# Kernel tuning notes

Measured on AMD Instinct MI355X. Metric: run time of the kernel, lower is better.

Reference implementation:

```python
import jax, jax.numpy as jnp
import numpy as np

D_MODEL = 1024
N_HEADS = 16
D_K = D_MODEL // N_HEADS


def setup_inputs() -> dict:
    key = jax.random.key(0)
    ks = jax.random.split(key, 16)
    B, S = 2, 2048
    sc = 1.0 / np.sqrt(D_MODEL)
    inp = {
        "query": jax.random.normal(ks[0], (B, S, D_MODEL), jnp.float32),
        "key": jax.random.normal(ks[1], (B, S, D_MODEL), jnp.float32),
        "value": jax.random.normal(ks[2], (B, S, D_MODEL), jnp.float32),
        "Wq": jax.random.normal(ks[3], (D_MODEL, D_MODEL), jnp.float32) * sc,
        "bq": jnp.zeros((D_MODEL,), jnp.float32),
        "Wk": jax.random.normal(ks[4], (D_MODEL, D_MODEL), jnp.float32) * sc,
        "bk": jnp.zeros((D_MODEL,), jnp.float32),
        "Wv": jax.random.normal(ks[5], (D_MODEL, D_MODEL), jnp.float32) * sc,
        "bv": jnp.zeros((D_MODEL,), jnp.float32),
        "Wo": jax.random.normal(ks[6], (D_MODEL, D_MODEL), jnp.float32) * sc,
        "bo": jnp.zeros((D_MODEL,), jnp.float32),
        "theta": jax.random.normal(ks[7], (N_HEADS,), jnp.float32) * 0.1,
        "gate": jax.random.normal(ks[8], (D_MODEL,), jnp.float32) * 0.1,
    }
    return inp


def reference(query, key, value, Wq, bq, Wk, bk, Wv, bv, Wo, bo, theta, gate):
    B, Sq, D = query.shape
    Sk = key.shape[1]
    # linear projections (torch Linear: x @ W.T + b), split heads -> [B,H,S,d_k]
    Q = (query @ Wq.T + bq).reshape(B, Sq, N_HEADS, D_K).transpose(0, 2, 1, 3)
    K = (key @ Wk.T + bk).reshape(B, Sk, N_HEADS, D_K).transpose(0, 2, 1, 3)
    V = (value @ Wv.T + bv).reshape(B, Sk, N_HEADS, D_K).transpose(0, 2, 1, 3)

    inv_sqrt_dk = 1.0 / jnp.sqrt(jnp.float32(D_K))
    scores = jnp.einsum("bhqd,bhkd->bhqk", Q, K) * inv_sqrt_dk

    # per-head rotation of the first two feature dims of Q
    cos_t = jnp.cos(theta)[None, :, None, None]  # [1,H,1,1]
    sin_t = jnp.sin(theta)[None, :, None, None]
    q_rot = jnp.concatenate(
        [
            cos_t * Q[..., :1] - sin_t * Q[..., 1:2],
            sin_t * Q[..., :1] + cos_t * Q[..., 1:2],
            Q[..., 2:],
        ],
        axis=-1,
    )
    scores_q = jnp.einsum("bhqd,bhkd->bhqk", q_rot, K) * inv_sqrt_dk

    g_scalar = jax.nn.sigmoid(gate.mean())
    scores = g_scalar * scores_q + (1.0 - g_scalar) * scores

    attn = jax.nn.softmax(scores, axis=-1)
    out = jnp.einsum("bhqk,bhkd->bhqd", attn, V)
    out = out.transpose(0, 2, 1, 3).reshape(B, Sq, D)
    return out @ Wo.T + bo
```

## Files before the change

### kernel.cpp

```cpp
#include <hip/hip_runtime.h>


typedef __bf16 bf16;
typedef __attribute__((ext_vector_type(8))) bf16 bf16x8;
typedef __attribute__((ext_vector_type(4))) bf16 bf16x4;
typedef __attribute__((ext_vector_type(2))) bf16 bf16x2;
typedef __attribute__((ext_vector_type(4))) float f32x4;
typedef unsigned int u32;

#define D_MODEL 1024
#define NH 16
#define DKH 64
#define SEQ 2048

#define GLL16(g, l) __builtin_amdgcn_global_load_lds(                      \
    (const __attribute__((address_space(1))) void*)(g),                    \
    (__attribute__((address_space(3))) void*)(l), 16, 0, 0)

static __device__ __forceinline__ f32x4 mfma16(bf16x8 a, bf16x8 b, f32x4 c) {
  return __builtin_amdgcn_mfma_f32_16x16x32_bf16(a, b, c, 0, 0, 0);
}

static __device__ __forceinline__ u32 pk2(float a, float b) {
  bf16x2 v; v[0] = (bf16)a; v[1] = (bf16)b;
  return __builtin_bit_cast(u32, v);
}

static __device__ __forceinline__ float fexp2(float x) {
#if __has_builtin(__builtin_amdgcn_exp2f)
  return __builtin_amdgcn_exp2f(x);
#else
  return exp2f(x);
#endif
}

#define CQK 0.1803368801111244f
#define MSHIFT 12.0f

__global__ __launch_bounds__(256) void prep(const float* __restrict__ query,
                                            const float* __restrict__ key,
                                            const float* __restrict__ value,
                                            const float* __restrict__ Wq,
                                            const float* __restrict__ bq,
                                            const float* __restrict__ Wk,
                                            const float* __restrict__ Wv,
                                            const float* __restrict__ Wo,
                                            const float* __restrict__ gate,
                                            const float* __restrict__ theta,
                                            bf16* __restrict__ Xq,
                                            bf16* __restrict__ Xk,
                                            bf16* __restrict__ Xv,
                                            bf16* __restrict__ Wqp,
                                            bf16* __restrict__ Wkp,
                                            bf16* __restrict__ Wvp,
                                            bf16* __restrict__ Wop,
                                            float* __restrict__ bqp) {
  const int id = blockIdx.x;
  const int tid = threadIdx.x;
  if (id >= 4096) {
    const int rem = id - 4096;
    const int iz = rem >> 12;
    const int ib = rem & 4095;
    const float* s = (iz == 0) ? query : (iz == 1) ? key : value;
    bf16* d = (iz == 0) ? Xq : (iz == 1) ? Xk : Xv;
    const size_t i = (size_t)(ib * 256 + tid) * 4;
    float4 w = *(const float4*)(s + i);
    bf16x4 o; o[0] = (bf16)w.x; o[1] = (bf16)w.y; o[2] = (bf16)w.z; o[3] = (bf16)w.w;
    *(bf16x4*)(d + i) = o;
    return;
  }
  const int wz = id >> 10, wb = id & 1023;
  if (wz != 0) {
    const float* s = (wz == 1) ? Wk : (wz == 2) ? Wv : Wo;
    bf16* dd = (wz == 1) ? Wkp : (wz == 2) ? Wvp : Wop;
    const size_t i = (size_t)(wb * 256 + tid) * 4;
    float4 v = *(const float4*)(s + i);
    bf16x4 o4; o4[0] = (bf16)v.x; o4[1] = (bf16)v.y; o4[2] = (bf16)v.z; o4[3] = (bf16)v.w;
    *(bf16x4*)(dd + i) = o4;
    return;
  }
  __shared__ float red[4];
  float ssum = 0.f;
  for (int i = tid; i < D_MODEL; i += 256) ssum += gate[i];
#pragma unroll
  for (int off = 32; off > 0; off >>= 1) ssum += __shfl_down(ssum, off);
  if ((tid & 63) == 0) red[tid >> 6] = ssum;
  __syncthreads();
  const float g = 1.f / (1.f + __expf(-(red[0] + red[1] + red[2] + red[3]) / 1024.f));

  const int t = wb * 256 + tid;
  const int r = t >> 8;
  const int c0 = (t & 255) * 4;
  const int d = r & 63, h = r >> 6;
  float4 w = *(const float4*)(Wq + (size_t)r * D_MODEL + c0);
  float4 o;
  if (d == 0) {
    const float a = (g * cosf(theta[h]) + (1.f - g)) * CQK;
    const float bb = (g * sinf(theta[h])) * CQK;
    float4 w2 = *(const float4*)(Wq + (size_t)(r + 1) * D_MODEL + c0);
    o.x = a * w.x - bb * w2.x; o.y = a * w.y - bb * w2.y;
    o.z = a * w.z - bb * w2.z; o.w = a * w.w - bb * w2.w;
    if (c0 == 0) bqp[r] = a * bq[r] - bb * bq[r + 1];
  } else if (d == 1) {
    const float a = (g * cosf(theta[h]) + (1.f - g)) * CQK;
    const float bb = (g * sinf(theta[h])) * CQK;
    float4 w2 = *(const float4*)(Wq + (size_t)(r - 1) * D_MODEL + c0);
    o.x = bb * w2.x + a * w.x; o.y = bb * w2.y + a * w.y;
    o.z = bb * w2.z + a * w.z; o.w = bb * w2.w + a * w.w;
    if (c0 == 0) bqp[r] = bb * bq[r - 1] + a * bq[r];
  } else {
    o.x = CQK * w.x; o.y = CQK * w.y;
    o.z = CQK * w.z; o.w = CQK * w.w;
    if (c0 == 0) bqp[r] = CQK * bq[r];
  }
  bf16x4 ov; ov[0] = (bf16)o.x; ov[1] = (bf16)o.y; ov[2] = (bf16)o.z; ov[3] = (bf16)o.w;
  *(bf16x4*)(Wqp + (size_t)r * D_MODEL + c0) = ov;
}

static __device__ __forceinline__ void gemm_bt_main(const bf16* __restrict__ A,
                                                    const bf16* __restrict__ Bt,
                                                    int tm, int tn, int K,
                                                    f32x4 acc[4][4]) {
  __shared__ bf16 lA[8192];
  __shared__ bf16 lB[8192];
  const int tid = threadIdx.x;
  const int lane = tid & 63, wv = tid >> 6;
  const int wm = wv >> 1, wn = wv & 1;
  const int l16 = lane & 15, lg = lane >> 4;

#pragma unroll
  for (int i = 0; i < 4; ++i)
#pragma unroll
    for (int j = 0; j < 4; ++j) acc[i][j] = (f32x4){0.f, 0.f, 0.f, 0.f};

  int offA[4][2], offB[4][2];
#pragma unroll
  for (int f = 0; f < 4; ++f)
#pragma unroll
    for (int kc = 0; kc < 2; ++kc) {
      const int m = wm * 64 + f * 16 + l16;
      offA[f][kc] = m * 64 + (((kc * 4 + lg) ^ (m & 7)) << 3);
      const int n = wn * 64 + f * 16 + l16;
      offB[f][kc] = n * 64 + (((kc * 4 + lg) ^ (n & 7)) << 3);
    }

  const int rowb = tid >> 3, oct = tid & 7;
  const int soct = oct ^ (rowb & 7);
  const bf16* gA[4];
  const bf16* gB[4];
#pragma unroll
  for (int rd = 0; rd < 4; ++rd) {
    gA[rd] = A + (size_t)(tm + rd * 32 + rowb) * K + soct * 8;
    gB[rd] = Bt + (size_t)(tn + rd * 32 + rowb) * K + soct * 8;
  }

  for (int kt = 0; kt < K; kt += 64) {
    __syncthreads();
#pragma unroll
    for (int rd = 0; rd < 4; ++rd) {
      GLL16(gA[rd] + kt, &lA[rd * 2048 + wv * 512]);
      GLL16(gB[rd] + kt, &lB[rd * 2048 + wv * 512]);
    }
    __syncthreads();
#pragma unroll
    for (int kc = 0; kc < 2; ++kc) {
      bf16x8 af[4], bv[4];
#pragma unroll
      for (int f = 0; f < 4; ++f) {
        af[f] = *(const bf16x8*)&lA[offA[f][kc]];
        bv[f] = *(const bf16x8*)&lB[offB[f][kc]];
      }
#pragma unroll
      for (int i = 0; i < 4; ++i)
#pragma unroll
        for (int j = 0; j < 4; ++j)
          acc[i][j] = mfma16(af[i], bv[j], acc[i][j]);
    }
  }
}

__global__ __launch_bounds__(256) void gemm_qkv(
    const bf16* __restrict__ Xq, const bf16* __restrict__ Xk, const bf16* __restrict__ Xv,
    const bf16* __restrict__ Wq, const bf16* __restrict__ Wk, const bf16* __restrict__ Wv,
    const float* __restrict__ bqp, const float* __restrict__ bk, const float* __restrict__ bv,
    bf16* __restrict__ Qp, bf16* __restrict__ Kp, bf16* __restrict__ Vt) {
  const int wgp = (blockIdx.x & 7) * 96 + (blockIdx.x >> 3);
  const int z = wgp >> 8;
  const int rem = wgp & 255;
  const int tm = (rem >> 3) * 128, tn = (rem & 7) * 128;
  const bf16* A = (z == 0) ? Xq : (z == 1) ? Xk : Xv;
  const bf16* Bt = (z == 0) ? Wq : (z == 1) ? Wk : Wv;
  const float* bias = (z == 0) ? bqp : (z == 1) ? bk : bv;
  f32x4 acc[4][4];
  gemm_bt_main(A, Bt, tm, tn, D_MODEL, acc);
  const int lane = threadIdx.x & 63, wv = threadIdx.x >> 6;
  const int wm = wv >> 1, wn = wv & 1, l16 = lane & 15, lg = lane >> 4;
  if (z < 2) {
    bf16* C = (z == 0) ? Qp : Kp;
#pragma unroll
    for (int i = 0; i < 4; ++i) {
      const int m0 = tm + wm * 64 + i * 16 + lg * 4;
#pragma unroll
      for (int j = 0; j < 4; ++j) {
        const int n = tn + wn * 64 + j * 16 + l16;
        const float bb = bias[n];
        const int h = n >> 6, d = n & 63;
#pragma unroll
        for (int r = 0; r < 4; ++r) {
          const int m = m0 + r;
          const int b = m >> 11, s = m & 2047;
          C[((size_t)(b * NH + h) * SEQ + s) * DKH + d] = (bf16)(acc[i][j][r] + bb);
        }
      }
    }
  } else {
#pragma unroll
    for (int i = 0; i < 4; ++i) {
      const int m0 = tm + wm * 64 + i * 16 + lg * 4;
      const int b = m0 >> 11, s0 = m0 & 2047;
#pragma unroll
      for (int j = 0; j < 4; ++j) {
        const int n = tn + wn * 64 + j * 16 + l16;
        const float bb = bias[n];
        const int h = n >> 6, d = n & 63;
        bf16x4 ov;
#pragma unroll
        for (int r = 0; r < 4; ++r) ov[r] = (bf16)(acc[i][j][r] + bb);
        *(bf16x4*)&Vt[((size_t)(b * NH + h) * DKH + d) * SEQ + s0] = ov;
      }
    }
  }
}

__global__ __launch_bounds__(256) void gemm_out_k(const bf16* __restrict__ A,
                                                  const bf16* __restrict__ Bt,
                                                  const float* __restrict__ bias,
                                                  float* __restrict__ C) {
  const int wgp = (blockIdx.x & 7) * 32 + (blockIdx.x >> 3);
  const int tm = (wgp >> 3) * 128, tn = (wgp & 7) * 128;
  f32x4 acc[4][4];
  gemm_bt_main(A, Bt, tm, tn, D_MODEL, acc);
  const int lane = threadIdx.x & 63, wv = threadIdx.x >> 6;
  const int wm = wv >> 1, wn = wv & 1, l16 = lane & 15, lg = lane >> 4;
#pragma unroll
  for (int i = 0; i < 4; ++i) {
    const int m0 = tm + wm * 64 + i * 16 + lg * 4;
#pragma unroll
    for (int j = 0; j < 4; ++j) {
      const int n = tn + wn * 64 + j * 16 + l16;
      const float bb = bias[n];
#pragma unroll
      for (int r = 0; r < 4; ++r)
        C[(size_t)(m0 + r) * D_MODEL + n] = acc[i][j][r] + bb;
    }
  }
}

__global__ __launch_bounds__(512, 4) void attn_kernel(const bf16* __restrict__ Qp,
                                                      const bf16* __restrict__ Kp,
                                                      const bf16* __restrict__ Vt,
                                                      bf16* __restrict__ Op) {
  __shared__ __align__(16) char smem[81920];
  bf16 (*lK)[8192] = (bf16(*)[8192])smem;
  bf16 (*lV)[8192] = (bf16(*)[8192])(smem + 32768);
  bf16* lP = (bf16*)(smem + 65536);
  float* cmb = (float*)smem;
  float* cl  = (float*)(smem + 65536);

  const int tid = threadIdx.x;
  const int lane = tid & 63, w = tid >> 6;
  const int l16 = lane & 15, lg = lane >> 4;
  const int qg = w >> 1, kg = w & 1;
  const int wgp = (blockIdx.x & 7) * 64 + (blockIdx.x >> 3);
  const int bh = wgp >> 4;
  const int b = bh >> 4, h = bh & 15;
  const int q0 = (wgp & 15) * 128;
  const int qw0 = q0 + qg * 32;
  const size_t kvb = (size_t)bh * SEQ * DKH;

  bf16x8 aq[2][2];
#pragma unroll
  for (int qq = 0; qq < 2; ++qq)
#pragma unroll
    for (int kc = 0; kc < 2; ++kc)
      aq[qq][kc] = *(const bf16x8*)&Qp[kvb +
          (size_t)(qw0 + qq * 16 + l16) * DKH + kc * 32 + lg * 8];

  f32x4 o[2][4];
#pragma unroll
  for (int qq = 0; qq < 2; ++qq)
#pragma unroll
    for (int dt = 0; dt < 4; ++dt) o[qq][dt] = (f32x4){0.f, 0.f, 0.f, 0.f};
  f32x4 lacc[2];
  lacc[0] = (f32x4){0.f, 0.f, 0.f, 0.f};
  lacc[1] = (f32x4){0.f, 0.f, 0.f, 0.f};

  bf16x8 ones;
#pragma unroll
  for (int j = 0; j < 8; ++j) ones[j] = (bf16)1.0f;

  const int kr = tid >> 3, oct = tid & 7;
  const bf16* gK = Kp + kvb + (size_t)kr * DKH + (oct ^ (kr & 7)) * 8;
  const int kswz0 = kr * 64 + (oct << 3);
  const int kswz1 = (kr + 64) * 64 + (oct << 3);
  const int vd = tid >> 4, vsc = tid & 15;
  const bf16* gV = Vt + kvb + (size_t)vd * SEQ + vsc * 8;
  const int vswz0 = vd * 128 + ((vsc ^ (vd & 7)) << 3);
  const int vswz1 = (vd + 32) * 128 + ((vsc ^ (vd & 7)) << 3);

  bf16* lPw = &lP[w * 1024];
  int pwr[2][2];
#pragma unroll
  for (int fn = 0; fn < 2; ++fn)
#pragma unroll
    for (int qq = 0; qq < 2; ++qq)
      pwr[fn][qq] = l16 * 64 + (((qq * 4 + fn * 2 + (lg >> 1)) ^ (l16 & 7)) << 3) +
                    ((lg & 1) << 2);
  int prd[2];
#pragma unroll
  for (int qq = 0; qq < 2; ++qq)
    prd[qq] = l16 * 64 + (((qq * 4 + lg) ^ (l16 & 7)) << 3);

  bf16x8 k0r = *(const bf16x8*)(gK);
  bf16x8 k1r = *(const bf16x8*)(gK + (size_t)64 * DKH);
  bf16x8 v0r = *(const bf16x8*)(gV);
  bf16x8 v1r = *(const bf16x8*)(gV + (size_t)32 * SEQ);
  *(bf16x8*)&lK[0][kswz0] = k0r;  *(bf16x8*)&lK[0][kswz1] = k1r;
  *(bf16x8*)&lV[0][vswz0] = v0r;  *(bf16x8*)&lV[0][vswz1] = v1r;
  k0r = *(const bf16x8*)(gK + (size_t)128 * DKH);
  k1r = *(const bf16x8*)(gK + (size_t)192 * DKH);
  v0r = *(const bf16x8*)(gV + 128);
  v1r = *(const bf16x8*)(gV + (size_t)32 * SEQ + 128);
  __syncthreads();

  const int NT = SEQ / 128;
  for (int t = 0; t < NT; ++t) {
    const bf16* K = &lK[t & 1][0];
    const bf16* V = &lV[t & 1][0];

#pragma unroll
    for (int ss = 0; ss < 2; ++ss) {
      f32x4 st[2][2];
      __builtin_amdgcn_s_setprio(1);
#pragma unroll
      for (int fn = 0; fn < 2; ++fn) {
        const int row = ss * 64 + kg * 32 + fn * 16 + l16;
        bf16x8 ka = *(const bf16x8*)&K[row * 64 + ((lg ^ (row & 7)) << 3)];
        bf16x8 kb = *(const bf16x8*)&K[row * 64 + (((4 + lg) ^ (row & 7)) << 3)];
#pragma unroll
        for (int qq = 0; qq < 2; ++qq) {
          f32x4 tt = (f32x4){0.f, 0.f, 0.f, 0.f};
          tt = mfma16(ka, aq[qq][0], tt);
          tt = mfma16(kb, aq[qq][1], tt);
          st[fn][qq] = tt;
        }
      }
      __builtin_amdgcn_s_setprio(0);

#pragma unroll
      for (int fn = 0; fn < 2; ++fn)
#pragma unroll
        for (int qq = 0; qq < 2; ++qq) {
          uint2 pw;
          pw.x = pk2(fexp2(st[fn][qq][0] - MSHIFT), fexp2(st[fn][qq][1] - MSHIFT));
          pw.y = pk2(fexp2(st[fn][qq][2] - MSHIFT), fexp2(st[fn][qq][3] - MSHIFT));
          *(uint2*)&lPw[pwr[fn][qq]] = pw;
        }

      bf16x8 pa0 = *(const bf16x8*)&lPw[prd[0]];
      bf16x8 pa1 = *(const bf16x8*)&lPw[prd[1]];

      __builtin_amdgcn_s_setprio(1);
      lacc[0] = mfma16(pa0, ones, lacc[0]);
      lacc[1] = mfma16(pa1, ones, lacc[1]);
#pragma unroll
      for (int dt = 0; dt < 4; ++dt) {
        const int n = dt * 16 + l16;
        bf16x8 vv = *(const bf16x8*)&V[n * 128 +
                                      (((ss * 8 + kg * 4 + lg) ^ (n & 7)) << 3)];
        o[0][dt] = mfma16(pa0, vv, o[0][dt]);
        o[1][dt] = mfma16(pa1, vv, o[1][dt]);
      }
      __builtin_amdgcn_s_setprio(0);
    }

    if (t + 1 < NT) {
      const int nb = (t + 1) & 1;
      *(bf16x8*)&lK[nb][kswz0] = k0r;  *(bf16x8*)&lK[nb][kswz1] = k1r;
      *(bf16x8*)&lV[nb][vswz0] = v0r;  *(bf16x8*)&lV[nb][vswz1] = v1r;
      if (t + 2 < NT) {
        const int kt2 = (t + 2) * 128;
        k0r = *(const bf16x8*)(gK + (size_t)kt2 * DKH);
        k1r = *(const bf16x8*)(gK + (size_t)(kt2 + 64) * DKH);
        v0r = *(const bf16x8*)(gV + kt2);
        v1r = *(const bf16x8*)(gV + (size_t)32 * SEQ + kt2);
      }
    }
    __syncthreads();
  }

  if (kg == 1) {
#pragma unroll
    for (int qq = 0; qq < 2; ++qq)
#pragma unroll
      for (int dt = 0; dt < 4; ++dt)
        *(f32x4*)&cmb[(size_t)qg * 2048 + ((qq * 4 + dt) * 16 + l16) * 16 + lg * 4] =
            o[qq][dt];
    if (l16 == 0) {
#pragma unroll
      for (int qq = 0; qq < 2; ++qq)
#pragma unroll
        for (int r = 0; r < 4; ++r)
          cl[(qg * 2 + qq) * 16 + lg * 4 + r] = lacc[qq][r];
    }
  }
  __syncthreads();
  if (kg == 0) {
#pragma unroll
    for (int qq = 0; qq < 2; ++qq) {
#pragma unroll
      for (int dt = 0; dt < 4; ++dt) {
        f32x4 p = *(const f32x4*)&cmb[(size_t)qg * 2048 +
                                      ((qq * 4 + dt) * 16 + l16) * 16 + lg * 4];
        o[qq][dt][0] += p[0]; o[qq][dt][1] += p[1];
        o[qq][dt][2] += p[2]; o[qq][dt][3] += p[3];
      }
      float linv[4];
#pragma unroll
      for (int r = 0; r < 4; ++r)
        linv[r] = 1.f / (lacc[qq][r] + cl[(qg * 2 + qq) * 16 + lg * 4 + r]);
#pragma unroll
      for (int r = 0; r < 4; ++r) {
        const int q = qw0 + qq * 16 + lg * 4 + r;
#pragma unroll
        for (int dt = 0; dt < 4; ++dt) {
          const int d = dt * 16 + l16;
          Op[((size_t)(b * SEQ + q)) * D_MODEL + h * DKH + d] =
              (bf16)(o[qq][dt][r] * linv[r]);
        }
      }
    }
  }
}

extern "C" void kernel_launch(void* const* d_in, const int* in_sizes, int n_in,
                              void* d_out, int out_size, void* d_ws, size_t ws_size,
                              hipStream_t stream) {
  (void)in_sizes; (void)n_in; (void)out_size; (void)ws_size;
  const float* query = (const float*)d_in[0];
  const float* key   = (const float*)d_in[1];
  const float* value = (const float*)d_in[2];
  const float* Wq    = (const float*)d_in[3];
  const float* bq    = (const float*)d_in[4];
  const float* Wk    = (const float*)d_in[5];
  const float* bk    = (const float*)d_in[6];
  const float* Wv    = (const float*)d_in[7];
  const float* bv    = (const float*)d_in[8];
  const float* Wo    = (const float*)d_in[9];
  const float* bo    = (const float*)d_in[10];
  const float* theta = (const float*)d_in[11];
  const float* gate  = (const float*)d_in[12];

  float* bqp = (float*)d_ws;
  bf16* wb = (bf16*)((char*)d_ws + 8192);
  bf16* Xq  = wb;
  bf16* Xk  = Xq + 4194304;
  bf16* Xv  = Xk + 4194304;
  bf16* Wqp = Xv + 4194304;
  bf16* Wkp = Wqp + 1048576;
  bf16* Wvp = Wkp + 1048576;
  bf16* Wop = Wvp + 1048576;
  bf16* Qp  = Wop + 1048576;
  bf16* Kp  = Qp + 4194304;
  bf16* Vt  = Kp + 4194304;
  bf16* Op  = Vt + 4194304;

  prep<<<16384, 256, 0, stream>>>(query, key, value, Wq, bq, Wk, Wv, Wo,
                                  gate, theta, Xq, Xk, Xv,
                                  Wqp, Wkp, Wvp, Wop, bqp);
  gemm_qkv<<<768, 256, 0, stream>>>(Xq, Xk, Xv, Wqp, Wkp, Wvp,
                                    bqp, bk, bv, Qp, Kp, Vt);
  attn_kernel<<<512, 512, 0, stream>>>(Qp, Kp, Vt, Op);
  gemm_out_k<<<256, 256, 0, stream>>>(Op, Wop, bo, (float*)d_out);
}
```

Baseline: 121.4 us.

## Stage attention K/V tiles via direct global-to-LDS loads with double buffering

Replaces the register-staged K/V prefetch, where global data was loaded into registers and then written to LDS, with global_load_lds direct copies into explicitly named double buffers. The swizzle moves from the LDS write address to the global read address, and the loop is unrolled by two so the buffers alternate without index arithmetic. The intent is to free VGPRs and remove the LDS write instructions, while relying on the async copy to overlap with compute. The epilogue combine buffers are remapped onto the new LDS arrays.

```diff
diff --git a/kernel.cpp b/kernel.cpp
--- a/kernel.cpp
+++ b/kernel.cpp
@@ -260,12 +260,11 @@
                                                       const bf16* __restrict__ Kp,
                                                       const bf16* __restrict__ Vt,
                                                       bf16* __restrict__ Op) {
-  __shared__ __align__(16) char smem[81920];
-  bf16 (*lK)[8192] = (bf16(*)[8192])smem;
-  bf16 (*lV)[8192] = (bf16(*)[8192])(smem + 32768);
-  bf16* lP = (bf16*)(smem + 65536);
-  float* cmb = (float*)smem;
-  float* cl  = (float*)(smem + 65536);
+  __shared__ __align__(16) bf16 lK0[8192];
+  __shared__ __align__(16) bf16 lV0[8192];
+  __shared__ __align__(16) bf16 lK1[8192];
+  __shared__ __align__(16) bf16 lV1[8192];
+  __shared__ __align__(16) bf16 lP[8192];
 
   const int tid = threadIdx.x;
   const int lane = tid & 63, w = tid >> 6;
@@ -300,13 +299,11 @@
   for (int j = 0; j < 8; ++j) ones[j] = (bf16)1.0f;
 
   const int kr = tid >> 3, oct = tid & 7;
-  const bf16* gK = Kp + kvb + (size_t)kr * DKH + (oct ^ (kr & 7)) * 8;
-  const int kswz0 = kr * 64 + (oct << 3);
-  const int kswz1 = (kr + 64) * 64 + (oct << 3);
+  const bf16* gKs = Kp + kvb + (size_t)kr * DKH + (oct ^ (kr & 7)) * 8;
+  const bf16* gKs2 = gKs + (size_t)64 * DKH;
   const int vd = tid >> 4, vsc = tid & 15;
-  const bf16* gV = Vt + kvb + (size_t)vd * SEQ + vsc * 8;
-  const int vswz0 = vd * 128 + ((vsc ^ (vd & 7)) << 3);
-  const int vswz1 = (vd + 32) * 128 + ((vsc ^ (vd & 7)) << 3);
+  const bf16* gVs = Vt + kvb + (size_t)vd * SEQ + ((vsc ^ (vd & 7)) * 8);
+  const bf16* gVs2 = gVs + (size_t)32 * SEQ;
 
   bf16* lPw = &lP[w * 1024];
   int pwr[2][2];
@@ -321,23 +318,16 @@
   for (int qq = 0; qq < 2; ++qq)
     prd[qq] = l16 * 64 + (((qq * 4 + lg) ^ (l16 & 7)) << 3);
 
-  bf16x8 k0r = *(const bf16x8*)(gK);
-  bf16x8 k1r = *(const bf16x8*)(gK + (size_t)64 * DKH);
-  bf16x8 v0r = *(const bf16x8*)(gV);
-  bf16x8 v1r = *(const bf16x8*)(gV + (size_t)32 * SEQ);
-  *(bf16x8*)&lK[0][kswz0] = k0r;  *(bf16x8*)&lK[0][kswz1] = k1r;
-  *(bf16x8*)&lV[0][vswz0] = v0r;  *(bf16x8*)&lV[0][vswz1] = v1r;
-  k0r = *(const bf16x8*)(gK + (size_t)128 * DKH);
-  k1r = *(const bf16x8*)(gK + (size_t)192 * DKH);
-  v0r = *(const bf16x8*)(gV + 128);
-  v1r = *(const bf16x8*)(gV + (size_t)32 * SEQ + 128);
-  __syncthreads();
-
-  const int NT = SEQ / 128;
-  for (int t = 0; t < NT; ++t) {
-    const bf16* K = &lK[t & 1][0];
-    const bf16* V = &lV[t & 1][0];
-
+  auto stageTile = [&](bf16* dK, bf16* dV, int t) {
+    const size_t ko = (size_t)t * 128 * DKH;
+    const int vo = t * 128;
+    GLL16(gKs + ko, dK + tid * 8);
+    GLL16(gKs2 + ko, dK + tid * 8 + 4096);
+    GLL16(gVs + vo, dV + tid * 8);
+    GLL16(gVs2 + vo, dV + tid * 8 + 4096);
+  };
+
+  auto computeTile = [&](const bf16* K, const bf16* V) {
 #pragma unroll
     for (int ss = 0; ss < 2; ++ss) {
       f32x4 st[2][2];
@@ -383,29 +373,31 @@
       }
       __builtin_amdgcn_s_setprio(0);
     }
-
-    if (t + 1 < NT) {
-      const int nb = (t + 1) & 1;
-      *(bf16x8*)&lK[nb][kswz0] = k0r;  *(bf16x8*)&lK[nb][kswz1] = k1r;
-      *(bf16x8*)&lV[nb][vswz0] = v0r;  *(bf16x8*)&lV[nb][vswz1] = v1r;
-      if (t + 2 < NT) {
-        const int kt2 = (t + 2) * 128;
-        k0r = *(const bf16x8*)(gK + (size_t)kt2 * DKH);
-        k1r = *(const bf16x8*)(gK + (size_t)(kt2 + 64) * DKH);
-        v0r = *(const bf16x8*)(gV + kt2);
-        v1r = *(const bf16x8*)(gV + (size_t)32 * SEQ + kt2);
-      }
-    }
+  };
+
+  stageTile(lK0, lV0, 0);
+  __syncthreads();
+
+  const int NT = SEQ / 128;
+  for (int t = 0; t < NT; t += 2) {
+    if (t + 1 < NT) stageTile(lK1, lV1, t + 1);
+    computeTile(lK0, lV0);
     __syncthreads();
-  }
-
+    if (t + 2 < NT) stageTile(lK0, lV0, t + 2);
+    computeTile(lK1, lV1);
+    __syncthreads();
+  }
+
+  float* cmb0 = (float*)lK0;
+  float* cmb1 = (float*)lK1;
+  float* cl = (float*)lP;
+  float* cmb = (qg < 2) ? (cmb0 + (size_t)qg * 2048) : (cmb1 + (size_t)(qg - 2) * 2048);
   if (kg == 1) {
 #pragma unroll
     for (int qq = 0; qq < 2; ++qq)
 #pragma unroll
       for (int dt = 0; dt < 4; ++dt)
-        *(f32x4*)&cmb[(size_t)qg * 2048 + ((qq * 4 + dt) * 16 + l16) * 16 + lg * 4] =
-            o[qq][dt];
+        *(f32x4*)&cmb[((qq * 4 + dt) * 16 + l16) * 16 + lg * 4] = o[qq][dt];
     if (l16 == 0) {
 #pragma unroll
       for (int qq = 0; qq < 2; ++qq)
@@ -420,8 +412,7 @@
     for (int qq = 0; qq < 2; ++qq) {
 #pragma unroll
       for (int dt = 0; dt < 4; ++dt) {
-        f32x4 p = *(const f32x4*)&cmb[(size_t)qg * 2048 +
-                                      ((qq * 4 + dt) * 16 + l16) * 16 + lg * 4];
+        f32x4 p = *(const f32x4*)&cmb[((qq * 4 + dt) * 16 + l16) * 16 + lg * 4];
         o[qq][dt][0] += p[0]; o[qq][dt][1] += p[1];
         o[qq][dt][2] += p[2]; o[qq][dt][3] += p[3];
       }
```

Result: no change. 121.2 us (median of 2 runs) (-0.2%).
